# Performance work log

Hardware: AMD Instinct MI355X
Metric: run time of the kernel (lower is better)

## Reference

```python
import jax, jax.numpy as jnp
import numpy as np

T, C, N, H = 60, 128, 4096, 128  # timesteps, channels(=hidden), pixel samples, hidden
GP = 5  # gp_affected_timesteps


def setup_inputs() -> dict:
    key = jax.random.key(0)
    k1, k2, k3 = jax.random.split(key, 3)
    s = 1.0 / np.sqrt(H)
    return {
        "image_stack": jax.random.normal(k1, (T, C, N), dtype=jnp.float32),
        "mask": jnp.zeros((T, N), dtype=jnp.float32),  # accepted but unused by original forward
        "W_ih": jax.random.uniform(k2, (4 * H, C), dtype=jnp.float32, minval=-s, maxval=s),
        "W_hh": jax.random.uniform(k3, (4 * H, H), dtype=jnp.float32, minval=-s, maxval=s),
        "b_ih": jnp.zeros((4 * H,), dtype=jnp.float32),
        "b_hh": jnp.zeros((4 * H,), dtype=jnp.float32),
        "gp_affected_timesteps": GP,
    }


def _lstm_cell(carry, xt, W_ih, W_hh, b):
    h, c = carry
    gates = xt @ W_ih.T + h @ W_hh.T + b  # [N, 4H]
    i, f, g, o = jnp.split(gates, 4, axis=-1)
    i, f, o = jax.nn.sigmoid(i), jax.nn.sigmoid(f), jax.nn.sigmoid(o)
    g = jnp.tanh(g)
    c = f * c + i * g
    h = o * jnp.tanh(c)
    return (h, c), h


def reference(image_stack, mask, W_ih, W_hh, b_ih, b_hh, gp_affected_timesteps):
    t, ch, n = image_stack.shape
    h = ch  # output fed back as input => hidden == channels
    b = b_ih + b_hh
    xs = jnp.transpose(image_stack, (0, 2, 1))  # [T, N, C]
    init = (jnp.zeros((n, h), image_stack.dtype), jnp.zeros((n, h), image_stack.dtype))

    cell = lambda carry, xt: _lstm_cell(carry, xt, W_ih, W_hh, b)
    carry, outs1 = jax.lax.scan(cell, init, xs)  # [T, N, H]

    extra = t - gp_affected_timesteps - 1
    ar = lambda carry, _: _lstm_cell(carry, carry[0], W_ih, W_hh, b)
    carry, outs2 = jax.lax.scan(ar, carry, None, length=extra)  # [extra, N, H]

    outs = jnp.concatenate([outs1, outs2], axis=0)  # [T+extra, N, H]
    return jnp.transpose(outs, (1, 0, 2))  # batch-first [N, T+extra, H]
```

## Files before the change

kernel.cpp:

```cpp
#include <hip/hip_runtime.h>
#include <hip/hip_bf16.h>

typedef __attribute__((ext_vector_type(8))) short short8;
typedef __attribute__((ext_vector_type(4))) float f32x4;

constexpr int T    = 60;
constexpr int C    = 128;
constexpr int NPIX = 4096;
constexpr int H    = 128;
constexpr int GP   = 5;
constexpr int EXTRA = T - GP - 1;
constexpr int TT    = T + EXTRA;
constexpr int LDS_STRIDE = 136;
constexpr int BUFE = 16 * LDS_STRIDE;
constexpr int OS_STRIDE = 132;
constexpr int OSB = 16 * OS_STRIDE;

__device__ __forceinline__ unsigned short f2bf(float f) {
  unsigned u = __float_as_uint(f);
  u += 0x7FFF + ((u >> 16) & 1);
  return (unsigned short)(u >> 16);
}
__device__ __forceinline__ float bf2f(unsigned short s) {
  return __uint_as_float(((unsigned)s) << 16);
}
__device__ __forceinline__ float fast_sigmoid(float x) {
  float e = __builtin_amdgcn_exp2f(-1.44269504f * x);
  return __builtin_amdgcn_rcpf(1.0f + e);
}
__device__ __forceinline__ float fast_tanh(float x) {
  float e = __builtin_amdgcn_exp2f(2.88539008f * x);
  return 1.0f - 2.0f * __builtin_amdgcn_rcpf(1.0f + e);
}

__device__ __forceinline__ void wg_barrier() {
  asm volatile("s_waitcnt lgkmcnt(0)" ::: "memory");
  __builtin_amdgcn_s_barrier();
  __builtin_amdgcn_sched_barrier(0);
}

__global__ __launch_bounds__(512, 2) void lstm_persistent(
    const float* __restrict__ img,
    const float* __restrict__ wih,
    const float* __restrict__ whh,
    const float* __restrict__ bih,
    const float* __restrict__ bhh,
    float* __restrict__ out)
{
  __shared__ __align__(16) unsigned short xs[2 * BUFE];
  __shared__ __align__(16) unsigned short hs[2 * BUFE];
  __shared__ __align__(16) float os[2 * OSB];

  const int tid  = threadIdx.x;
  const int lane = tid & 63;
  const int w    = tid >> 6;
  const int l15  = lane & 15;
  const int quad = lane >> 4;
  const int lb   = ((int)blockIdx.x & 7) * 32 + ((int)blockIdx.x >> 3);
  const int n0   = lb * 16;
  const int hid  = w * 16 + l15;

  short8 fih[4][4], fhh[4][4];
  float bias[4];
  #pragma unroll
  for (int nt = 0; nt < 4; ++nt) {
    const int col = nt * 128 + hid;
    bias[nt] = bih[col] + bhh[col];
    #pragma unroll
    for (int kt = 0; kt < 4; ++kt) {
      const int k0 = kt * 32 + quad * 8;
      const float* pih = wih + col * C + k0;
      const float* phh = whh + col * C + k0;
      short8 a, b;
      #pragma unroll
      for (int j = 0; j < 8; ++j) {
        a[j] = (short)f2bf(pih[j]);
        b[j] = (short)f2bf(phh[j]);
      }
      fih[nt][kt] = a;
      fhh[nt][kt] = b;
    }
  }

  for (int i = tid; i < BUFE; i += 512) hs[i] = 0;

  float c[4] = {0.f, 0.f, 0.f, 0.f};

  const int nl = tid & 15;
  const int cb = (tid >> 4) * 4;
  const float* xbase = img + (size_t)cb * NPIX + n0 + nl;

  auto loadx = [&](int t) -> f32x4 {
    const float* p = xbase + (size_t)t * (C * NPIX);
    return (f32x4){p[0], p[NPIX], p[2 * NPIX], p[3 * NPIX]};
  };

  {
    f32x4 q = loadx(0);
    ushort4 pk;
    pk.x = f2bf(q[0]); pk.y = f2bf(q[1]); pk.z = f2bf(q[2]); pk.w = f2bf(q[3]);
    *(ushort4*)&xs[nl * LDS_STRIDE + cb] = pk;
  }
  f32x4 qcur = loadx(1);
  wg_barrier();

  const int fro = l15 * LDS_STRIDE + quad * 8;

  const int ss = tid >> 5;
  const int c4 = (tid & 31) * 4;
  const size_t obs = (size_t)TT * H;
  float* osp = out + (size_t)(n0 + ss) * obs + c4;

  auto step_drv = [&](int so, int dso, int oso, bool wx, f32x4 qx) {
    f32x4 acc[4];
    #pragma unroll
    for (int nt = 0; nt < 4; ++nt)
      acc[nt] = (f32x4){bias[nt], bias[nt], bias[nt], bias[nt]};
    #pragma unroll
    for (int kt = 0; kt < 4; ++kt) {
      short8 ax = *(const short8*)&xs[so + fro + kt * 32];
      short8 ah = *(const short8*)&hs[so + fro + kt * 32];
      #pragma unroll
      for (int nt = 0; nt < 4; ++nt) {
        acc[nt] = __builtin_amdgcn_mfma_f32_16x16x32_bf16(ax, fih[nt][kt], acc[nt], 0, 0, 0);
        acc[nt] = __builtin_amdgcn_mfma_f32_16x16x32_bf16(ah, fhh[nt][kt], acc[nt], 0, 0, 0);
      }
    }
    if (wx) {
      ushort4 pk;
      pk.x = f2bf(qx[0]); pk.y = f2bf(qx[1]); pk.z = f2bf(qx[2]); pk.w = f2bf(qx[3]);
      *(ushort4*)&xs[dso + nl * LDS_STRIDE + cb] = pk;
    }
    float hv[4];
    #pragma unroll
    for (int r = 0; r < 4; ++r) {
      float ig = fast_sigmoid(acc[0][r]);
      float fg = fast_sigmoid(acc[1][r]);
      float gg = fast_tanh(acc[2][r]);
      float og = fast_sigmoid(acc[3][r]);
      c[r] = fg * c[r] + ig * gg;
      hv[r] = og * fast_tanh(c[r]);
    }
    #pragma unroll
    for (int r = 0; r < 4; ++r) {
      hs[dso + (quad * 4 + r) * LDS_STRIDE + hid] = f2bf(hv[r]);
      os[oso + (quad * 4 + r) * OS_STRIDE + hid] = hv[r];
    }
    wg_barrier();
    {
      f32x4 v = *(const f32x4*)&os[oso + ss * OS_STRIDE + c4];
      __builtin_nontemporal_store(v, (f32x4*)osp);
      osp += H;
    }
  };

  auto step_ar = [&](int so, int dso, int oso) {
    f32x4 acc[4];
    #pragma unroll
    for (int nt = 0; nt < 4; ++nt)
      acc[nt] = (f32x4){bias[nt], bias[nt], bias[nt], bias[nt]};
    #pragma unroll
    for (int kt = 0; kt < 4; ++kt) {
      short8 ah = *(const short8*)&hs[so + fro + kt * 32];
      #pragma unroll
      for (int nt = 0; nt < 4; ++nt)
        acc[nt] = __builtin_amdgcn_mfma_f32_16x16x32_bf16(ah, fih[nt][kt], acc[nt], 0, 0, 0);
    }
    float hv[4];
    #pragma unroll
    for (int r = 0; r < 4; ++r) {
      float ig = fast_sigmoid(acc[0][r]);
      float fg = fast_sigmoid(acc[1][r]);
      float gg = fast_tanh(acc[2][r]);
      float og = fast_sigmoid(acc[3][r]);
      c[r] = fg * c[r] + ig * gg;
      hv[r] = og * fast_tanh(c[r]);
    }
    #pragma unroll
    for (int r = 0; r < 4; ++r) {
      hs[dso + (quad * 4 + r) * LDS_STRIDE + hid] = f2bf(hv[r]);
      os[oso + (quad * 4 + r) * OS_STRIDE + hid] = hv[r];
    }
    wg_barrier();
    {
      f32x4 v = *(const f32x4*)&os[oso + ss * OS_STRIDE + c4];
      __builtin_nontemporal_store(v, (f32x4*)osp);
      osp += H;
    }
  };

  #pragma unroll 1
  for (int t = 0; t < T - 4; t += 2) {
    f32x4 qA = loadx(t + 2);
    step_drv(0, BUFE, OSB, true, qcur);
    f32x4 qB = loadx(t + 3);
    step_drv(BUFE, 0, 0, true, qA);
    qcur = qB;
  }
  {
    f32x4 qA = loadx(58);
    step_drv(0, BUFE, OSB, true, qcur);
    f32x4 qB = loadx(59);
    step_drv(BUFE, 0, 0, true, qA);
    qcur = qB;
  }
  {
    step_drv(0, BUFE, OSB, true, qcur);
    step_drv(BUFE, 0, 0, false, qcur);
  }

  #pragma unroll
  for (int nt = 0; nt < 4; ++nt)
    #pragma unroll
    for (int kt = 0; kt < 4; ++kt) {
      short8 a = fih[nt][kt], b = fhh[nt][kt];
      #pragma unroll
      for (int j = 0; j < 8; ++j)
        a[j] = (short)f2bf(bf2f((unsigned short)a[j]) + bf2f((unsigned short)b[j]));
      fih[nt][kt] = a;
    }

  #pragma unroll 1
  for (int t = 0; t < EXTRA; t += 2) {
    step_ar(0, BUFE, OSB);
    step_ar(BUFE, 0, 0);
  }
}

extern "C" void kernel_launch(void* const* d_in, const int* in_sizes, int n_in,
                              void* d_out, int out_size, void* d_ws, size_t ws_size,
                              hipStream_t stream) {
  (void)in_sizes; (void)n_in; (void)d_ws; (void)ws_size; (void)out_size;
  const float* img = (const float*)d_in[0];
  const float* wih = (const float*)d_in[2];
  const float* whh = (const float*)d_in[3];
  const float* bih = (const float*)d_in[4];
  const float* bhh = (const float*)d_in[5];
  float* out = (float*)d_out;

  lstm_persistent<<<NPIX / 16, 512, 0, stream>>>(img, wih, whh, bih, bhh, out);
}
```

Measured before the change: 525.0 us.

## Halve pixels per block to 8 and double grid for more occupancy

Each workgroup now handles 8 pixel samples instead of 16, so the grid has twice as many blocks and launch bounds request 4 blocks per CU. MFMA tiles stay 16 rows wide: rows 8-15 duplicate rows 0-7, and only the first two quads write results. The barrier now also drains outstanding global memory ops. The aim is to fill the GPU better on the latency-bound recurrence, at the cost of doing half-redundant MFMA work per block and carrying register pressure under the higher occupancy target.

```diff
diff --git a/kernel.cpp b/kernel.cpp
--- a/kernel.cpp
+++ b/kernel.cpp
@@ -3,6 +3,7 @@
 
 typedef __attribute__((ext_vector_type(8))) short short8;
 typedef __attribute__((ext_vector_type(4))) float f32x4;
+typedef __attribute__((ext_vector_type(2))) float f32x2;
 
 constexpr int T    = 60;
 constexpr int C    = 128;
@@ -11,10 +12,11 @@
 constexpr int GP   = 5;
 constexpr int EXTRA = T - GP - 1;
 constexpr int TT    = T + EXTRA;
+constexpr int SAMP  = 8;
 constexpr int LDS_STRIDE = 136;
-constexpr int BUFE = 16 * LDS_STRIDE;
+constexpr int BUFE = SAMP * LDS_STRIDE;
 constexpr int OS_STRIDE = 132;
-constexpr int OSB = 16 * OS_STRIDE;
+constexpr int OSB = SAMP * OS_STRIDE;
 
 __device__ __forceinline__ unsigned short f2bf(float f) {
   unsigned u = __float_as_uint(f);
@@ -33,13 +35,13 @@
   return 1.0f - 2.0f * __builtin_amdgcn_rcpf(1.0f + e);
 }
 
-__device__ __forceinline__ void wg_barrier() {
-  asm volatile("s_waitcnt lgkmcnt(0)" ::: "memory");
+__device__ __forceinline__ void wg_barrier_drain() {
+  asm volatile("s_waitcnt vmcnt(0) lgkmcnt(0)" ::: "memory");
   __builtin_amdgcn_s_barrier();
   __builtin_amdgcn_sched_barrier(0);
 }
 
-__global__ __launch_bounds__(512, 2) void lstm_persistent(
+__global__ __launch_bounds__(512, 4) void lstm_persistent(
     const float* __restrict__ img,
     const float* __restrict__ wih,
     const float* __restrict__ whh,
@@ -56,8 +58,8 @@
   const int w    = tid >> 6;
   const int l15  = lane & 15;
   const int quad = lane >> 4;
-  const int lb   = ((int)blockIdx.x & 7) * 32 + ((int)blockIdx.x >> 3);
-  const int n0   = lb * 16;
+  const int lb   = ((int)blockIdx.x & 7) * 64 + ((int)blockIdx.x >> 3);
+  const int n0   = lb * SAMP;
   const int hid  = w * 16 + l15;
 
   short8 fih[4][4], fhh[4][4];
@@ -86,32 +88,33 @@
 
   float c[4] = {0.f, 0.f, 0.f, 0.f};
 
-  const int nl = tid & 15;
-  const int cb = (tid >> 4) * 4;
+  const int nl = tid & 7;
+  const int cb = (tid >> 3) * 2;
   const float* xbase = img + (size_t)cb * NPIX + n0 + nl;
 
-  auto loadx = [&](int t) -> f32x4 {
+  auto loadx = [&](int t) -> f32x2 {
     const float* p = xbase + (size_t)t * (C * NPIX);
-    return (f32x4){p[0], p[NPIX], p[2 * NPIX], p[3 * NPIX]};
+    return (f32x2){p[0], p[NPIX]};
   };
 
   {
-    f32x4 q = loadx(0);
-    ushort4 pk;
-    pk.x = f2bf(q[0]); pk.y = f2bf(q[1]); pk.z = f2bf(q[2]); pk.w = f2bf(q[3]);
-    *(ushort4*)&xs[nl * LDS_STRIDE + cb] = pk;
-  }
-  f32x4 qcur = loadx(1);
-  wg_barrier();
-
-  const int fro = l15 * LDS_STRIDE + quad * 8;
-
-  const int ss = tid >> 5;
-  const int c4 = (tid & 31) * 4;
+    f32x2 q = loadx(0);
+    ushort2 pk; pk.x = f2bf(q[0]); pk.y = f2bf(q[1]);
+    *(ushort2*)&xs[nl * LDS_STRIDE + cb] = pk;
+  }
+  f32x2 qcur = loadx(1);
+
+  const int fro = (l15 & 7) * LDS_STRIDE + quad * 8;
+  const bool wr = (quad < 2);
+
+  const int ss = tid >> 6;
+  const int c2 = (tid & 63) * 2;
   const size_t obs = (size_t)TT * H;
-  float* osp = out + (size_t)(n0 + ss) * obs + c4;
-
-  auto step_drv = [&](int so, int dso, int oso, bool wx, f32x4 qx) {
+  float* osp = out + (size_t)(n0 + ss) * obs + c2;
+
+  wg_barrier_drain();
+
+  auto step_drv = [&](int so, int dso, int oso, bool wx, f32x2 qx) {
     f32x4 acc[4];
     #pragma unroll
     for (int nt = 0; nt < 4; ++nt)
@@ -127,9 +130,8 @@
       }
     }
     if (wx) {
-      ushort4 pk;
-      pk.x = f2bf(qx[0]); pk.y = f2bf(qx[1]); pk.z = f2bf(qx[2]); pk.w = f2bf(qx[3]);
-      *(ushort4*)&xs[dso + nl * LDS_STRIDE + cb] = pk;
+      ushort2 pk; pk.x = f2bf(qx[0]); pk.y = f2bf(qx[1]);
+      *(ushort2*)&xs[dso + nl * LDS_STRIDE + cb] = pk;
     }
     float hv[4];
     #pragma unroll
@@ -141,17 +143,17 @@
       c[r] = fg * c[r] + ig * gg;
       hv[r] = og * fast_tanh(c[r]);
     }
-    #pragma unroll
-    for (int r = 0; r < 4; ++r) {
-      hs[dso + (quad * 4 + r) * LDS_STRIDE + hid] = f2bf(hv[r]);
-      os[oso + (quad * 4 + r) * OS_STRIDE + hid] = hv[r];
-    }
-    wg_barrier();
-    {
-      f32x4 v = *(const f32x4*)&os[oso + ss * OS_STRIDE + c4];
-      __builtin_nontemporal_store(v, (f32x4*)osp);
-      osp += H;
-    }
+    if (wr) {
+      #pragma unroll
+      for (int r = 0; r < 4; ++r) {
+        hs[dso + (quad * 4 + r) * LDS_STRIDE + hid] = f2bf(hv[r]);
+        os[oso + (quad * 4 + r) * OS_STRIDE + hid] = hv[r];
+      }
+    }
+    wg_barrier_drain();
+    f32x2 v = *(const f32x2*)&os[oso + ss * OS_STRIDE + c2];
+    __builtin_nontemporal_store(v, (f32x2*)osp);
+    osp += H;
   };
 
   auto step_ar = [&](int so, int dso, int oso) {
@@ -176,31 +178,31 @@
       c[r] = fg * c[r] + ig * gg;
       hv[r] = og * fast_tanh(c[r]);
     }
-    #pragma unroll
-    for (int r = 0; r < 4; ++r) {
-      hs[dso + (quad * 4 + r) * LDS_STRIDE + hid] = f2bf(hv[r]);
-      os[oso + (quad * 4 + r) * OS_STRIDE + hid] = hv[r];
-    }
-    wg_barrier();
-    {
-      f32x4 v = *(const f32x4*)&os[oso + ss * OS_STRIDE + c4];
-      __builtin_nontemporal_store(v, (f32x4*)osp);
-      osp += H;
-    }
+    if (wr) {
+      #pragma unroll
+      for (int r = 0; r < 4; ++r) {
+        hs[dso + (quad * 4 + r) * LDS_STRIDE + hid] = f2bf(hv[r]);
+        os[oso + (quad * 4 + r) * OS_STRIDE + hid] = hv[r];
+      }
+    }
+    wg_barrier_drain();
+    f32x2 v = *(const f32x2*)&os[oso + ss * OS_STRIDE + c2];
+    __builtin_nontemporal_store(v, (f32x2*)osp);
+    osp += H;
   };
 
   #pragma unroll 1
   for (int t = 0; t < T - 4; t += 2) {
-    f32x4 qA = loadx(t + 2);
+    f32x2 qA = loadx(t + 2);
     step_drv(0, BUFE, OSB, true, qcur);
-    f32x4 qB = loadx(t + 3);
+    f32x2 qB = loadx(t + 3);
     step_drv(BUFE, 0, 0, true, qA);
     qcur = qB;
   }
   {
-    f32x4 qA = loadx(58);
+    f32x2 qA = loadx(58);
     step_drv(0, BUFE, OSB, true, qcur);
-    f32x4 qB = loadx(59);
+    f32x2 qB = loadx(59);
     step_drv(BUFE, 0, 0, true, qA);
     qcur = qB;
   }
@@ -238,5 +240,5 @@
   const float* bhh = (const float*)d_in[5];
   float* out = (float*)d_out;
 
-  lstm_persistent<<<NPIX / 16, 512, 0, stream>>>(img, wih, whh, bih, bhh, out);
-}
+  lstm_persistent<<<NPIX / SAMP, 512, 0, stream>>>(img, wih, whh, bih, bhh, out);
+}
```

After: 1.508 ms. +187.2%, slower.
